# Performance work log

Hardware: AMD Instinct MI355X
Metric: run time of the kernel (lower is better)

The kernel has to match this reference:

```python
import jax, jax.numpy as jnp
import numpy as np

N = 100000      # nodes
E = 300000      # edges
D_IN = 256
D_HID = 128
K = 2           # num_concat
L = 8           # num_layer
C = 40          # num_class
CH = K * D_HID  # GCNII channels = 256
ALPHA = 0.1
THETA = 0.5


def setup_inputs() -> dict:
    key = jax.random.key(0)
    ks = jax.random.split(key, 8)
    return {
        "x0": jax.random.normal(ks[0], (N, D_IN), dtype=jnp.float32),
        "x1": jax.random.normal(ks[1], (N, D_IN), dtype=jnp.float32),
        "edge_index": jax.random.randint(ks[2], (2, E), 0, N, dtype=jnp.int32),
        "lin_w": jax.random.normal(ks[3], (K, D_IN, D_HID), dtype=jnp.float32) * 0.05,
        "lin_b": jnp.zeros((K, D_HID), dtype=jnp.float32),
        "gcn_w": jax.random.normal(ks[4], (L, CH, CH), dtype=jnp.float32) * 0.05,
        "out_w": jax.random.normal(ks[5], (CH, C), dtype=jnp.float32) * 0.05,
        "out_b": jnp.zeros((C,), dtype=jnp.float32),
    }


def reference(x0, x1, edge_index, lin_w, lin_b, gcn_w, out_w, out_b):
    # per-view linear + relu, then concat -> h_0   [N, CH]
    h0 = jnp.concatenate(
        [jax.nn.relu(x0 @ lin_w[0] + lin_b[0]),
         jax.nn.relu(x1 @ lin_w[1] + lin_b[1])], axis=-1)

    src, dst = edge_index[0], edge_index[1]
    # GCN2Conv beta for layer l (1-indexed): log(theta/l + 1)
    betas = jnp.log(THETA / jnp.arange(1, L + 1, dtype=jnp.float32) + 1.0)

    def step(h, wb):
        w, beta = wb
        # propagate (normalize=False): unweighted sum of source features at dst
        agg = jax.ops.segment_sum(h[src], dst, num_segments=N)  # [N, CH]
        x = (1.0 - ALPHA) * agg + ALPHA * h0                    # initial residual
        out = (1.0 - beta) * x + beta * (x @ w)                 # identity mapping
        return jax.nn.relu(out), None

    h, _ = jax.lax.scan(step, h0, (gcn_w, betas))
    return h @ out_w + out_b
```

## Files before the change

### kernel.cpp

```cpp
#include <hip/hip_runtime.h>
#include <cmath>


#define N_NODES 100000
#define N_EDGES 300000
#define DIN 256
#define CHN 256
#define DHID 128
#define NCLASS 40
#define NLAYER 8
#define SCAN_NB 98

typedef short bf16x8 __attribute__((ext_vector_type(8)));
typedef float f32x4 __attribute__((ext_vector_type(4)));

__device__ inline short f2bf(float f) {
  unsigned u = __float_as_uint(f);
  unsigned r = (u + 0x7FFFu + ((u >> 16) & 1u)) >> 16;
  return (short)r;
}
__device__ inline float bf2f(short s) {
  return __uint_as_float(((unsigned)(unsigned short)s) << 16);
}

__global__ void hist_kernel(const int* __restrict__ dst, int* __restrict__ cnt) {
  int e = blockIdx.x * 256 + threadIdx.x;
  if (e < N_EDGES) atomicAdd(&cnt[dst[e]], 1);
}

__global__ __launch_bounds__(256) void bscan1(const int* __restrict__ cnt,
                                              int* __restrict__ rowp,
                                              int* __restrict__ bsums) {
  int tid = threadIdx.x;
  int base = blockIdx.x * 1024 + tid * 4;
  int v0 = 0, v1 = 0, v2 = 0, v3 = 0;
  if (base + 3 < N_NODES) {
    int4 v = *(const int4*)(cnt + base);
    v0 = v.x; v1 = v.y; v2 = v.z; v3 = v.w;
  } else {
    if (base + 0 < N_NODES) v0 = cnt[base + 0];
    if (base + 1 < N_NODES) v1 = cnt[base + 1];
    if (base + 2 < N_NODES) v2 = cnt[base + 2];
    if (base + 3 < N_NODES) v3 = cnt[base + 3];
  }
  int t = v0 + v1 + v2 + v3;
  int lane = tid & 63;
  int incl = t;
#pragma unroll
  for (int off = 1; off < 64; off <<= 1) {
    int x = __shfl_up(incl, off, 64);
    if (lane >= off) incl += x;
  }
  __shared__ int wsum[4];
  int wave = tid >> 6;
  if (lane == 63) wsum[wave] = incl;
  __syncthreads();
  int woff = 0;
  for (int w = 0; w < wave; w++) woff += wsum[w];
  int excl = woff + incl - t;
  int e0 = excl, e1 = e0 + v0, e2 = e1 + v1, e3 = e2 + v2;
  if (base + 0 < N_NODES) rowp[base + 0] = e0;
  if (base + 1 < N_NODES) rowp[base + 1] = e1;
  if (base + 2 < N_NODES) rowp[base + 2] = e2;
  if (base + 3 < N_NODES) rowp[base + 3] = e3;
  if (tid == 255) bsums[blockIdx.x] = woff + incl;
}

__global__ void bscan2(int* __restrict__ bsums, int* __restrict__ rowp) {
  if (threadIdx.x == 0 && blockIdx.x == 0) {
    int s = 0;
    for (int i = 0; i < SCAN_NB; i++) {
      int v = bsums[i];
      bsums[i] = s;
      s += v;
    }
    rowp[N_NODES] = s;
  }
}

__global__ __launch_bounds__(256) void bscan3(int* __restrict__ rowp,
                                              int* __restrict__ fill,
                                              const int* __restrict__ bsums) {
  int base = blockIdx.x * 1024 + threadIdx.x * 4;
  int off = bsums[blockIdx.x];
#pragma unroll
  for (int j = 0; j < 4; j++) {
    int i = base + j;
    if (i < N_NODES) {
      int p = rowp[i] + off;
      rowp[i] = p;
      fill[i] = p;
    }
  }
}

__global__ void scatter_kernel(const int* __restrict__ src, const int* __restrict__ dst,
                               int* __restrict__ fill, int* __restrict__ col) {
  int e = blockIdx.x * 256 + threadIdx.x;
  if (e < N_EDGES) {
    int p = atomicAdd(&fill[dst[e]], 1);
    col[p] = src[e];
  }
}

__global__ void prep_w_kernel(const float* __restrict__ lw, const float* __restrict__ gw,
                              short* __restrict__ linT, short* __restrict__ gcnT) {
  int i = blockIdx.x * 256 + threadIdx.x;
  if (i < 2 * 128 * 256) {
    int v = i >> 15;
    int rem = i & 32767;
    int n = rem >> 8;
    int k = rem & 255;
    linT[i] = f2bf(lw[v * (DIN * DHID) + k * DHID + n]);
  }
  int j = i - 2 * 128 * 256;
  if (j >= 0 && j < 8 * 256 * 256) {
    int l = j >> 16;
    int rem = j & 65535;
    int n = rem >> 8;
    int k = rem & 255;
    gcnT[j] = f2bf(gw[l * (CHN * CHN) + k * CHN + n]);
  }
}

__global__ __launch_bounds__(256) void lin_mfma_kernel(const float* __restrict__ x0,
                                                       const float* __restrict__ x1,
                                                       const short* __restrict__ linT,
                                                       const float* __restrict__ lb,
                                                       short* __restrict__ h0) {
  const int view = blockIdx.y;
  const float* __restrict__ X = view ? x1 : x0;
  const short* __restrict__ Wt = linT + view * (DHID * DIN);
  const int row0 = blockIdx.x * 128;
  const int tid = threadIdx.x;
  const int lane = tid & 63, wave = tid >> 6;
  const int quad = lane >> 4, mrem = lane & 15;
  const int wrow = (wave & 1) * 64, wcol = (wave >> 1) * 64;

  f32x4 acc[4][4];
#pragma unroll
  for (int i = 0; i < 4; i++)
#pragma unroll
    for (int j = 0; j < 4; j++) acc[i][j] = (f32x4){0.f, 0.f, 0.f, 0.f};

  for (int k0 = 0; k0 < DIN; k0 += 32) {
    bf16x8 af[4], bfr[4];
#pragma unroll
    for (int j = 0; j < 4; j++)
      bfr[j] = *(const bf16x8*)(Wt + (size_t)(wcol + j * 16 + mrem) * DIN + k0 + quad * 8);
#pragma unroll
    for (int i = 0; i < 4; i++) {
      const int gr = row0 + wrow + i * 16 + mrem;
      float v[8];
      if (gr < N_NODES) {
        const float* p = X + (size_t)gr * DIN + k0 + quad * 8;
        *(float4*)(v + 0) = *(const float4*)(p + 0);
        *(float4*)(v + 4) = *(const float4*)(p + 4);
      } else {
#pragma unroll
        for (int q = 0; q < 8; q++) v[q] = 0.f;
      }
      short s[8];
#pragma unroll
      for (int q = 0; q < 8; q++) s[q] = f2bf(v[q]);
      af[i] = *(const bf16x8*)s;
    }
#pragma unroll
    for (int i = 0; i < 4; i++)
#pragma unroll
      for (int j = 0; j < 4; j++)
        acc[i][j] = __builtin_amdgcn_mfma_f32_16x16x32_bf16(af[i], bfr[j], acc[i][j], 0, 0, 0);
  }
#pragma unroll
  for (int i = 0; i < 4; i++) {
#pragma unroll
    for (int j = 0; j < 4; j++) {
      int lcol = wcol + j * 16 + mrem;
      float bb = lb[view * DHID + lcol];
#pragma unroll
      for (int r = 0; r < 4; r++) {
        int grow = row0 + wrow + i * 16 + quad * 4 + r;
        if (grow < N_NODES)
          h0[(size_t)grow * CHN + view * DHID + lcol] = f2bf(fmaxf(acc[i][j][r] + bb, 0.f));
      }
    }
  }
}

__global__ __launch_bounds__(512, 6) void layer_fused(const short* __restrict__ h,
                                                      const short* __restrict__ h0,
                                                      const int* __restrict__ rowp,
                                                      const int* __restrict__ col,
                                                      const short* __restrict__ Wt,
                                                      short* __restrict__ out, float beta) {
  __shared__ short As[64 * 264];
  const int tid = threadIdx.x;
  const int row0 = blockIdx.x * 64;

  const int t16 = tid & 15;
  const int team = tid >> 4;

  float acc[2][16];
#pragma unroll
  for (int p = 0; p < 2; p++)
#pragma unroll
    for (int q = 0; q < 16; q++) acc[p][q] = 0.f;

  int begs[2], dcnt[2];
  int maxd = 0;
#pragma unroll
  for (int p = 0; p < 2; p++) {
    const int gr = row0 + p * 32 + team;
    if (gr < N_NODES) {
      begs[p] = rowp[gr];
      dcnt[p] = rowp[gr + 1] - begs[p];
    } else {
      begs[p] = 0;
      dcnt[p] = 0;
    }
    maxd = max(maxd, dcnt[p]);
  }

  int scur[2];
#pragma unroll
  for (int p = 0; p < 2; p++) scur[p] = (0 < dcnt[p]) ? col[begs[p]] : -1;

  for (int i = 0; i < maxd; ++i) {
    int snxt[2];
#pragma unroll
    for (int p = 0; p < 2; p++) snxt[p] = (i + 1 < dcnt[p]) ? col[begs[p] + i + 1] : -1;
#pragma unroll
    for (int p = 0; p < 2; p++) {
      const int s = scur[p];
      if (s >= 0) {
        const short* hp = h + (size_t)s * CHN + t16 * 16;
        bf16x8 v0 = *(const bf16x8*)hp;
        bf16x8 v1 = *(const bf16x8*)(hp + 8);
#pragma unroll
        for (int q = 0; q < 8; q++) {
          acc[p][q] += bf2f(v0[q]);
          acc[p][q + 8] += bf2f(v1[q]);
        }
      }
    }
#pragma unroll
    for (int p = 0; p < 2; p++) scur[p] = snxt[p];
  }

#pragma unroll
  for (int p = 0; p < 2; p++) {
    const int r = p * 32 + team;
    const int gr = row0 + r;
    if (gr < N_NODES) {
      const short* p0 = h0 + (size_t)gr * CHN + t16 * 16;
      bf16x8 r0 = *(const bf16x8*)p0;
      bf16x8 r1 = *(const bf16x8*)(p0 + 8);
      short o[16];
#pragma unroll
      for (int q = 0; q < 8; q++) {
        o[q] = f2bf(0.9f * acc[p][q] + 0.1f * bf2f(r0[q]));
        o[q + 8] = f2bf(0.9f * acc[p][q + 8] + 0.1f * bf2f(r1[q]));
      }
      *(bf16x8*)&As[r * 264 + t16 * 16] = *(bf16x8*)o;
      *(bf16x8*)&As[r * 264 + t16 * 16 + 8] = *(bf16x8*)(o + 8);
    } else {
      bf16x8 z = (bf16x8)(short)0;
      *(bf16x8*)&As[r * 264 + t16 * 16] = z;
      *(bf16x8*)&As[r * 264 + t16 * 16 + 8] = z;
    }
  }
  __syncthreads();

  const int lane = tid & 63, wave = tid >> 6;
  const int quad = lane >> 4, mrem = lane & 15;
  const int wrow = (wave >> 2) * 32;
  const int wcol = (wave & 3) * 64;
  f32x4 acc2[2][4];
#pragma unroll
  for (int i = 0; i < 2; i++)
#pragma unroll
    for (int j = 0; j < 4; j++) acc2[i][j] = (f32x4){0.f, 0.f, 0.f, 0.f};

  for (int k0 = 0; k0 < CHN; k0 += 32) {
    bf16x8 af[2], bfr[4];
#pragma unroll
    for (int j = 0; j < 4; j++)
      bfr[j] = *(const bf16x8*)(Wt + (size_t)(wcol + j * 16 + mrem) * CHN + k0 + quad * 8);
#pragma unroll
    for (int i = 0; i < 2; i++)
      af[i] = *(const bf16x8*)&As[(wrow + i * 16 + mrem) * 264 + k0 + quad * 8];
#pragma unroll
    for (int i = 0; i < 2; i++)
#pragma unroll
      for (int j = 0; j < 4; j++)
        acc2[i][j] = __builtin_amdgcn_mfma_f32_16x16x32_bf16(af[i], bfr[j], acc2[i][j], 0, 0, 0);
  }

  const float omb = 1.f - beta;
#pragma unroll
  for (int i = 0; i < 2; i++) {
#pragma unroll
    for (int j = 0; j < 4; j++) {
      const int lcol = wcol + j * 16 + mrem;
#pragma unroll
      for (int r = 0; r < 4; r++) {
        const int lrow = wrow + i * 16 + quad * 4 + r;
        const int grow = row0 + lrow;
        if (grow < N_NODES) {
          float xv = bf2f(As[lrow * 264 + lcol]);
          out[(size_t)grow * CHN + lcol] = f2bf(fmaxf(omb * xv + beta * acc2[i][j][r], 0.f));
        }
      }
    }
  }
}

__global__ __launch_bounds__(256) void out_kernel(const short* __restrict__ h,
                                                  const float* __restrict__ W,
                                                  const float* __restrict__ b,
                                                  float* __restrict__ out) {
  __shared__ float xs[32][260];
  __shared__ float ws[64][40];
  const int row0 = blockIdx.x * 32;
  const int tid = threadIdx.x;
  for (int f = tid; f < 1024; f += 256) {
    int r = f >> 5;
    int c = (f & 31) * 8;
    bf16x8 v = *(const bf16x8*)(h + (size_t)(row0 + r) * CHN + c);
    float t0[8];
#pragma unroll
    for (int q = 0; q < 8; q++) t0[q] = bf2f(v[q]);
    *(float4*)&xs[r][c] = *(float4*)(t0);
    *(float4*)&xs[r][c + 4] = *(float4*)(t0 + 4);
  }
  const int r = tid >> 3;
  const int cg = (tid & 7) * 5;
  float acc[5];
#pragma unroll
  for (int j = 0; j < 5; j++) acc[j] = b[cg + j];
  for (int k0 = 0; k0 < CHN; k0 += 64) {
    for (int i = tid; i < 64 * 40; i += 256) {
      int k = i / 40, c = i % 40;
      ws[k][c] = W[(size_t)(k0 + k) * NCLASS + c];
    }
    __syncthreads();
#pragma unroll 8
    for (int k = 0; k < 64; k++) {
      float xv = xs[r][k0 + k];
#pragma unroll
      for (int j = 0; j < 5; j++) acc[j] += xv * ws[k][cg + j];
    }
    __syncthreads();
  }
  float* op = out + (size_t)(row0 + r) * NCLASS + cg;
#pragma unroll
  for (int j = 0; j < 5; j++) op[j] = acc[j];
}

extern "C" void kernel_launch(void* const* d_in, const int* in_sizes, int n_in,
                              void* d_out, int out_size, void* d_ws, size_t ws_size,
                              hipStream_t stream) {
  const float* x0 = (const float*)d_in[0];
  const float* x1 = (const float*)d_in[1];
  const int* ei = (const int*)d_in[2];
  const float* lw = (const float*)d_in[3];
  const float* lb = (const float*)d_in[4];
  const float* gw = (const float*)d_in[5];
  const float* ow = (const float*)d_in[6];
  const float* ob = (const float*)d_in[7];
  float* outp = (float*)d_out;

  const size_t NC = (size_t)N_NODES * CHN;
  short* h0 = (short*)d_ws;
  short* hb = h0 + NC;
  short* xb = hb + NC;
  short* linT = xb + NC;
  short* gcnT = linT + 2 * DHID * DIN;
  int* cnt = (int*)(gcnT + 8 * CHN * CHN);
  int* rowp = cnt + N_NODES;
  int* fill = rowp + N_NODES + 1;
  int* col = fill + N_NODES;
  int* bsums = col + N_EDGES;

  const int* src = ei;
  const int* dst = ei + N_EDGES;

  hipMemsetAsync(cnt, 0, N_NODES * sizeof(int), stream);
  hist_kernel<<<(N_EDGES + 255) / 256, 256, 0, stream>>>(dst, cnt);
  bscan1<<<SCAN_NB, 256, 0, stream>>>(cnt, rowp, bsums);
  bscan2<<<1, 64, 0, stream>>>(bsums, rowp);
  bscan3<<<SCAN_NB, 256, 0, stream>>>(rowp, fill, bsums);
  scatter_kernel<<<(N_EDGES + 255) / 256, 256, 0, stream>>>(src, dst, fill, col);
  prep_w_kernel<<<(2 * 128 * 256 + 8 * 256 * 256 + 255) / 256, 256, 0, stream>>>(lw, gw, linT, gcnT);

  dim3 lg((N_NODES + 127) / 128, 2);
  lin_mfma_kernel<<<lg, 256, 0, stream>>>(x0, x1, linT, lb, h0);

  const short* hin = h0;
  for (int l = 0; l < NLAYER; ++l) {
    float beta = logf(0.5f / (float)(l + 1) + 1.0f);
    short* hout = (l & 1) ? xb : hb;
    layer_fused<<<(N_NODES + 63) / 64, 512, 0, stream>>>(hin, h0, rowp, col,
                                                         gcnT + (size_t)l * CHN * CHN,
                                                         hout, beta);
    hin = hout;
  }
  out_kernel<<<N_NODES / 32, 256, 0, stream>>>(hin, ow, ob, outp);
}
```

Before: 1.135 ms.

## Remap lin and layer kernels: per-wave row tiles, 4-row gather, column-split MFMA

The linear kernel now gives each wave its own 64-row strip and splits output columns across grid y. Each wave then loads all of its own X rows, and X is read twice, once per column half. The fused layer kernel has each 32-lane team gather 8 channels for 4 rows at once, issuing four independent loads per step for more memory-level parallelism. Its MFMA stage now has each wave cover all 64 rows for 32 columns, which cuts redundant weight fetches per wave but adds more LDS A-fragment reads. The edge gather dominates the runtime, so the gather restructuring is the main intended win.

```diff
diff --git a/kernel.cpp b/kernel.cpp
--- a/kernel.cpp
+++ b/kernel.cpp
@@ -128,14 +128,15 @@
                                                        const short* __restrict__ linT,
                                                        const float* __restrict__ lb,
                                                        short* __restrict__ h0) {
-  const int view = blockIdx.y;
+  const int y = blockIdx.y;
+  const int view = y >> 1;
   const float* __restrict__ X = view ? x1 : x0;
   const short* __restrict__ Wt = linT + view * (DHID * DIN);
-  const int row0 = blockIdx.x * 128;
+  const int wcol = (y & 1) * 64;
   const int tid = threadIdx.x;
   const int lane = tid & 63, wave = tid >> 6;
   const int quad = lane >> 4, mrem = lane & 15;
-  const int wrow = (wave & 1) * 64, wcol = (wave >> 1) * 64;
+  const int row0 = blockIdx.x * 256 + wave * 64;
 
   f32x4 acc[4][4];
 #pragma unroll
@@ -150,7 +151,7 @@
       bfr[j] = *(const bf16x8*)(Wt + (size_t)(wcol + j * 16 + mrem) * DIN + k0 + quad * 8);
 #pragma unroll
     for (int i = 0; i < 4; i++) {
-      const int gr = row0 + wrow + i * 16 + mrem;
+      const int gr = row0 + i * 16 + mrem;
       float v[8];
       if (gr < N_NODES) {
         const float* p = X + (size_t)gr * DIN + k0 + quad * 8;
@@ -179,7 +180,7 @@
       float bb = lb[view * DHID + lcol];
 #pragma unroll
       for (int r = 0; r < 4; r++) {
-        int grow = row0 + wrow + i * 16 + quad * 4 + r;
+        int grow = row0 + i * 16 + quad * 4 + r;
         if (grow < N_NODES)
           h0[(size_t)grow * CHN + view * DHID + lcol] = f2bf(fmaxf(acc[i][j][r] + bb, 0.f));
       }
@@ -197,114 +198,100 @@
   const int tid = threadIdx.x;
   const int row0 = blockIdx.x * 64;
 
-  const int t16 = tid & 15;
-  const int team = tid >> 4;
-
-  float acc[2][16];
-#pragma unroll
-  for (int p = 0; p < 2; p++)
-#pragma unroll
-    for (int q = 0; q < 16; q++) acc[p][q] = 0.f;
-
-  int begs[2], dcnt[2];
-  int maxd = 0;
-#pragma unroll
-  for (int p = 0; p < 2; p++) {
-    const int gr = row0 + p * 32 + team;
+  const int c8 = (tid & 31) * 8;
+  const int rb = tid >> 5;
+
+  float acc[4][8];
+#pragma unroll
+  for (int p = 0; p < 4; p++)
+#pragma unroll
+    for (int q = 0; q < 8; q++) acc[p][q] = 0.f;
+
+  int beg[4], cnt[4];
+#pragma unroll
+  for (int p = 0; p < 4; p++) {
+    const int gr = row0 + rb + p * 16;
     if (gr < N_NODES) {
-      begs[p] = rowp[gr];
-      dcnt[p] = rowp[gr + 1] - begs[p];
+      beg[p] = rowp[gr];
+      cnt[p] = rowp[gr + 1] - beg[p];
     } else {
-      begs[p] = 0;
-      dcnt[p] = 0;
-    }
-    maxd = max(maxd, dcnt[p]);
-  }
-
-  int scur[2];
-#pragma unroll
-  for (int p = 0; p < 2; p++) scur[p] = (0 < dcnt[p]) ? col[begs[p]] : -1;
+      beg[p] = 0;
+      cnt[p] = 0;
+    }
+  }
+  const int maxd = max(max(cnt[0], cnt[1]), max(cnt[2], cnt[3]));
+
+  int scur[4];
+#pragma unroll
+  for (int p = 0; p < 4; p++) scur[p] = (cnt[p] > 0) ? col[beg[p]] : -1;
 
   for (int i = 0; i < maxd; ++i) {
-    int snxt[2];
-#pragma unroll
-    for (int p = 0; p < 2; p++) snxt[p] = (i + 1 < dcnt[p]) ? col[begs[p] + i + 1] : -1;
-#pragma unroll
-    for (int p = 0; p < 2; p++) {
-      const int s = scur[p];
-      if (s >= 0) {
-        const short* hp = h + (size_t)s * CHN + t16 * 16;
-        bf16x8 v0 = *(const bf16x8*)hp;
-        bf16x8 v1 = *(const bf16x8*)(hp + 8);
-#pragma unroll
-        for (int q = 0; q < 8; q++) {
-          acc[p][q] += bf2f(v0[q]);
-          acc[p][q + 8] += bf2f(v1[q]);
-        }
-      }
-    }
-#pragma unroll
-    for (int p = 0; p < 2; p++) scur[p] = snxt[p];
-  }
-
-#pragma unroll
-  for (int p = 0; p < 2; p++) {
-    const int r = p * 32 + team;
+    int snxt[4];
+#pragma unroll
+    for (int p = 0; p < 4; p++) snxt[p] = (i + 1 < cnt[p]) ? col[beg[p] + i + 1] : -1;
+    bf16x8 v[4];
+#pragma unroll
+    for (int p = 0; p < 4; p++)
+      v[p] = (scur[p] >= 0) ? *(const bf16x8*)(h + (size_t)scur[p] * CHN + c8)
+                            : (bf16x8)(short)0;
+#pragma unroll
+    for (int p = 0; p < 4; p++)
+#pragma unroll
+      for (int q = 0; q < 8; q++) acc[p][q] += bf2f(v[p][q]);
+#pragma unroll
+    for (int p = 0; p < 4; p++) scur[p] = snxt[p];
+  }
+
+#pragma unroll
+  for (int p = 0; p < 4; p++) {
+    const int r = rb + p * 16;
     const int gr = row0 + r;
+    short o[8];
     if (gr < N_NODES) {
-      const short* p0 = h0 + (size_t)gr * CHN + t16 * 16;
-      bf16x8 r0 = *(const bf16x8*)p0;
-      bf16x8 r1 = *(const bf16x8*)(p0 + 8);
-      short o[16];
-#pragma unroll
-      for (int q = 0; q < 8; q++) {
-        o[q] = f2bf(0.9f * acc[p][q] + 0.1f * bf2f(r0[q]));
-        o[q + 8] = f2bf(0.9f * acc[p][q + 8] + 0.1f * bf2f(r1[q]));
-      }
-      *(bf16x8*)&As[r * 264 + t16 * 16] = *(bf16x8*)o;
-      *(bf16x8*)&As[r * 264 + t16 * 16 + 8] = *(bf16x8*)(o + 8);
+      bf16x8 r0 = *(const bf16x8*)(h0 + (size_t)gr * CHN + c8);
+#pragma unroll
+      for (int q = 0; q < 8; q++) o[q] = f2bf(0.9f * acc[p][q] + 0.1f * bf2f(r0[q]));
     } else {
-      bf16x8 z = (bf16x8)(short)0;
-      *(bf16x8*)&As[r * 264 + t16 * 16] = z;
-      *(bf16x8*)&As[r * 264 + t16 * 16 + 8] = z;
-    }
+#pragma unroll
+      for (int q = 0; q < 8; q++) o[q] = 0;
+    }
+    *(bf16x8*)&As[r * 264 + c8] = *(bf16x8*)o;
   }
   __syncthreads();
 
   const int lane = tid & 63, wave = tid >> 6;
   const int quad = lane >> 4, mrem = lane & 15;
-  const int wrow = (wave >> 2) * 32;
-  const int wcol = (wave & 3) * 64;
-  f32x4 acc2[2][4];
-#pragma unroll
-  for (int i = 0; i < 2; i++)
-#pragma unroll
-    for (int j = 0; j < 4; j++) acc2[i][j] = (f32x4){0.f, 0.f, 0.f, 0.f};
+  const int wcol = wave * 32;
+  f32x4 acc2[4][2];
+#pragma unroll
+  for (int i = 0; i < 4; i++)
+#pragma unroll
+    for (int j = 0; j < 2; j++) acc2[i][j] = (f32x4){0.f, 0.f, 0.f, 0.f};
 
   for (int k0 = 0; k0 < CHN; k0 += 32) {
-    bf16x8 af[2], bfr[4];
-#pragma unroll
-    for (int j = 0; j < 4; j++)
+    bf16x8 af[4], bfr[2];
+#pragma unroll
+    for (int j = 0; j < 2; j++)
       bfr[j] = *(const bf16x8*)(Wt + (size_t)(wcol + j * 16 + mrem) * CHN + k0 + quad * 8);
 #pragma unroll
-    for (int i = 0; i < 2; i++)
-      af[i] = *(const bf16x8*)&As[(wrow + i * 16 + mrem) * 264 + k0 + quad * 8];
-#pragma unroll
-    for (int i = 0; i < 2; i++)
-#pragma unroll
-      for (int j = 0; j < 4; j++)
+    for (int i = 0; i < 4; i++)
+      af[i] = *(const bf16x8*)&As[(i * 16 + mrem) * 264 + k0 + quad * 8];
+#pragma unroll
+    for (int i = 0; i < 4; i++)
+#pragma unroll
+      for (int j = 0; j < 2; j++)
         acc2[i][j] = __builtin_amdgcn_mfma_f32_16x16x32_bf16(af[i], bfr[j], acc2[i][j], 0, 0, 0);
   }
 
   const float omb = 1.f - beta;
 #pragma unroll
-  for (int i = 0; i < 2; i++) {
-#pragma unroll
-    for (int j = 0; j < 4; j++) {
+  for (int i = 0; i < 4; i++) {
+#pragma unroll
+    for (int j = 0; j < 2; j++) {
       const int lcol = wcol + j * 16 + mrem;
 #pragma unroll
       for (int r = 0; r < 4; r++) {
-        const int lrow = wrow + i * 16 + quad * 4 + r;
+        const int lrow = i * 16 + quad * 4 + r;
         const int grow = row0 + lrow;
         if (grow < N_NODES) {
           float xv = bf2f(As[lrow * 264 + lcol]);
@@ -393,7 +380,7 @@
   scatter_kernel<<<(N_EDGES + 255) / 256, 256, 0, stream>>>(src, dst, fill, col);
   prep_w_kernel<<<(2 * 128 * 256 + 8 * 256 * 256 + 255) / 256, 256, 0, stream>>>(lw, gw, linT, gcnT);
 
-  dim3 lg((N_NODES + 127) / 128, 2);
+  dim3 lg((N_NODES + 255) / 256, 4);
   lin_mfma_kernel<<<lg, 256, 0, stream>>>(x0, x1, linT, lb, h0);
 
   const short* hin = h0;
```

After: 995.4 us. 1.14x faster.
